# Kernel tuning notes

Hardware: AMD Instinct MI355X
Metric: run time of the kernel (lower is better)

## Reference

```python
import jax, jax.numpy as jnp
import numpy as np

D_MODEL = 1024
D_STATE = 16
D_CONV = 4
EXPAND = 2
D_INNER = EXPAND * D_MODEL
BATCH = 2
SEQ = 4096


def setup_inputs() -> dict:
    key = jax.random.key(0)
    ks = jax.random.split(key, 8)
    def w(k, shape, fan_in):
        return jax.random.normal(k, shape, jnp.float32) * (fan_in ** -0.5)
    x = jax.random.normal(ks[0], (BATCH, SEQ, D_MODEL), jnp.float32)
    in_proj_w = w(ks[1], (2 * D_INNER, D_MODEL), D_MODEL)
    conv_w = w(ks[2], (D_INNER, 1, D_CONV), D_CONV)          # depthwise conv kernel (OIH, groups=D_INNER)
    conv_b = jnp.zeros((D_INNER,), jnp.float32)
    x_proj_w = w(ks[3], (1 + 2 * D_STATE, D_INNER), D_INNER)
    dt_proj_w = w(ks[4], (D_INNER, 1), D_STATE)               # Linear(1 -> d_inner), see notes
    dt_proj_b = jnp.zeros((D_INNER,), jnp.float32)
    A_log = jnp.log(jnp.tile(jnp.arange(1, D_STATE + 1, dtype=jnp.float32)[None, :], (D_INNER, 1)))
    D = jnp.ones((D_INNER,), jnp.float32)
    out_proj_w = w(ks[5], (D_MODEL, D_INNER), D_INNER)
    return dict(x=x, in_proj_w=in_proj_w, conv_w=conv_w, conv_b=conv_b,
                x_proj_w=x_proj_w, dt_proj_w=dt_proj_w, dt_proj_b=dt_proj_b,
                A_log=A_log, D=D, out_proj_w=out_proj_w)


def _selective_scan(xs, delta, Bm, Cm, A, D):
    # xs, delta: [B, L, d_inner]; Bm, Cm: [B, L, d_state]; A: [d_inner, d_state]
    def step(h, inp):
        x_t, d_t, b_t, c_t = inp                      # [B,di],[B,di],[B,n],[B,n]
        dA = jnp.exp(d_t[..., None] * A)              # [B, di, n]
        h = dA * h + (d_t * x_t)[..., None] * b_t[:, None, :]
        y = jnp.einsum('bdn,bn->bd', h, c_t) + D * x_t
        return h, y
    h0 = jnp.zeros((xs.shape[0], xs.shape[2], A.shape[1]), xs.dtype)
    seq = (jnp.swapaxes(xs, 0, 1), jnp.swapaxes(delta, 0, 1),
           jnp.swapaxes(Bm, 0, 1), jnp.swapaxes(Cm, 0, 1))
    _, ys = jax.lax.scan(step, h0, seq)               # ys: [L, B, di]
    return jnp.swapaxes(ys, 0, 1)


def _mamba(x, in_proj_w, conv_w, conv_b, x_proj_w, dt_proj_w, dt_proj_b, A_log, D, out_proj_w):
    xz = x @ in_proj_w.T                               # [B, L, 2*di]
    xc, z = jnp.split(xz, 2, axis=-1)
    # causal depthwise conv (pad left d_conv-1, truncate to seq_len)
    u = jnp.swapaxes(xc, 1, 2)                         # [B, di, L]
    u = jax.lax.conv_general_dilated(
        u, conv_w, window_strides=(1,), padding=[(D_CONV - 1, 0)],
        feature_group_count=D_INNER, dimension_numbers=('NCH', 'OIH', 'NCH'))
    u = u + conv_b[None, :, None]
    xs = jax.nn.silu(jnp.swapaxes(u, 1, 2))            # [B, L, di]
    dbc = xs @ x_proj_w.T                              # [B, L, 1+2n]
    delta_raw = dbc[..., :1]
    Bm = dbc[..., 1:1 + D_STATE]
    Cm = dbc[..., 1 + D_STATE:]
    delta = jax.nn.softplus(delta_raw @ dt_proj_w.T + dt_proj_b)   # [B, L, di]
    A = -jnp.exp(A_log)
    y = _selective_scan(xs, delta, Bm, Cm, A, D)
    return (y * jax.nn.silu(z)) @ out_proj_w.T


def reference(x, in_proj_w, conv_w, conv_b, x_proj_w, dt_proj_w, dt_proj_b, A_log, D, out_proj_w):
    return _mamba(x, in_proj_w, conv_w, conv_b, x_proj_w, dt_proj_w, dt_proj_b, A_log, D, out_proj_w)
```

## Files before the change

kernel.cpp:

```cpp
#include <hip/hip_runtime.h>
#include <hip/hip_bf16.h>
#include <stdint.h>

typedef __bf16 bf16x8 __attribute__((ext_vector_type(8)));
typedef float  f32x4  __attribute__((ext_vector_type(4)));
typedef float  f32x2  __attribute__((ext_vector_type(2)));
typedef unsigned short u16x8 __attribute__((ext_vector_type(8)));

#define TC 32
#define NC 128
#define TH 16

__device__ __forceinline__ unsigned short f2bf(float f) {
  unsigned u = __builtin_bit_cast(unsigned, f);
  unsigned r = (u + 0x7fffu + ((u >> 16) & 1u)) >> 16;
  return (unsigned short)r;
}
__device__ __forceinline__ float bf2f(unsigned short s) {
  unsigned u = ((unsigned)s) << 16;
  return __builtin_bit_cast(float, u);
}

__device__ __forceinline__ void gload_lds16(const void* g, void* l) {
  __builtin_amdgcn_global_load_lds(
      (const __attribute__((address_space(1))) unsigned int*)(g),
      (__attribute__((address_space(3))) unsigned int*)(l),
      16, 0, 0);
}

__global__ __launch_bounds__(256) void prep_k(
    const float4* __restrict__ x, const float4* __restrict__ ipw,
    const float4* __restrict__ opw, const float* __restrict__ xpw,
    ushort4* __restrict__ xb, ushort4* __restrict__ wb1,
    ushort4* __restrict__ wb2, unsigned short* __restrict__ xwp)
{
  const int r = blockIdx.y;
  int i = blockIdx.x * 256 + threadIdx.x;
  const int stride = gridDim.x * 256;
  if (r == 0) {
    for (; i < 2097152; i += stride) {
      float4 v = x[i]; ushort4 o;
      o.x = f2bf(v.x); o.y = f2bf(v.y); o.z = f2bf(v.z); o.w = f2bf(v.w);
      xb[i] = o;
    }
  } else if (r == 1) {
    for (; i < 1048576; i += stride) {
      float4 v = ipw[i]; ushort4 o;
      o.x = f2bf(v.x); o.y = f2bf(v.y); o.z = f2bf(v.z); o.w = f2bf(v.w);
      wb1[i] = o;
    }
  } else if (r == 2) {
    for (; i < 524288; i += stride) {
      float4 v = opw[i]; ushort4 o;
      o.x = f2bf(v.x); o.y = f2bf(v.y); o.z = f2bf(v.z); o.w = f2bf(v.w);
      wb2[i] = o;
    }
  } else {
    for (; i < 262144; i += stride) {
      int row = i >> 11, col = i & 2047;
      xwp[i] = (row < 33) ? f2bf(xpw[row * 2048 + col]) : (unsigned short)0;
    }
  }
}

template <bool BF16OUT, bool SWZ>
__global__ __launch_bounds__(512) void gemm8p(
    const unsigned short* __restrict__ A, const unsigned short* __restrict__ B,
    void* __restrict__ Cv, int M, int N, int K)
{
  __shared__ __align__(16) unsigned short As[2][2][8192];
  __shared__ __align__(16) unsigned short Bs[2][2][8192];
  const int tid = threadIdx.x;

  const int grid_m = M >> 8, grid_n = N >> 8;
  const int nwg = grid_m * grid_n;
  int wid = blockIdx.x;
  if (SWZ) { int q = nwg >> 3; wid = (wid & 7) * q + (wid >> 3); }
  const int GM = 8;
  const int nig = GM * grid_n;
  const int gidg = wid / nig;
  const int rem = wid - gidg * nig;
  const int fm = gidg * GM;
  const int gsz = (grid_m - fm < GM) ? (grid_m - fm) : GM;
  const int pm = fm + rem % gsz;
  const int pn = rem / gsz;
  const int m0 = pm << 8, n0 = pn << 8;

  const int NT = K >> 6;

  const int wq = tid >> 6, l = tid & 63;
  const int wr2 = wq >> 2, wc2 = wq & 3;
  const int lr = l & 15, q16 = l >> 4;
  const int sw = lr & 7;

  const unsigned short* aH0 = A + (size_t)m0 * K;
  const unsigned short* aH1 = A + (size_t)(m0 + 128) * K;
  const unsigned short* bH0 = B + (size_t)n0 * K;
  const unsigned short* bH1 = B + (size_t)(n0 + 128) * K;

#define STAGE8(srcbase, dstp, kt)                                              \
  { _Pragma("unroll") for (int i = 0; i < 2; ++i) {                            \
      int q = tid + 512 * i; int rw = q >> 3; int ssl = (q & 7) ^ (rw & 7);    \
      gload_lds16((srcbase) + (size_t)rw * K + (size_t)(kt) * 64 + ssl * 8,    \
                  (dstp) + q * 8); } }

#define LDA(dd, MH)                                                            \
  { _Pragma("unroll") for (int mi = 0; mi < 4; ++mi) {                         \
      int ar = (wr2 * 64 + mi * 16 + lr) * 64;                                 \
      _Pragma("unroll") for (int ks = 0; ks < 2; ++ks)                         \
        af[mi][ks] = *(const bf16x8*)&As[dd][MH][ar + (((ks * 4 + q16) ^ sw) << 3)]; } }

#define LDB(dd, NH)                                                            \
  { _Pragma("unroll") for (int ni = 0; ni < 2; ++ni) {                         \
      int br = (wc2 * 32 + ni * 16 + lr) * 64;                                 \
      _Pragma("unroll") for (int ks = 0; ks < 2; ++ks)                         \
        bf2[NH][ni][ks] = *(const bf16x8*)&Bs[dd][NH][br + (((ks * 4 + q16) ^ sw) << 3)]; } }

#define MMA(MH, NH)                                                            \
  { __builtin_amdgcn_s_setprio(1);                                             \
    _Pragma("unroll") for (int mi = 0; mi < 4; ++mi)                           \
    _Pragma("unroll") for (int ni = 0; ni < 2; ++ni)                           \
    _Pragma("unroll") for (int ks = 0; ks < 2; ++ks)                           \
      acc[MH][NH][mi][ni] = __builtin_amdgcn_mfma_f32_16x16x32_bf16(           \
          af[mi][ks], bf2[NH][ni][ks], acc[MH][NH][mi][ni], 0, 0, 0);          \
    __builtin_amdgcn_s_setprio(0); }

  f32x4 acc[2][2][4][2];
#pragma unroll
  for (int a = 0; a < 2; ++a)
#pragma unroll
    for (int b = 0; b < 2; ++b)
#pragma unroll
      for (int c = 0; c < 4; ++c)
#pragma unroll
        for (int d = 0; d < 2; ++d)
          acc[a][b][c][d] = (f32x4){0.f, 0.f, 0.f, 0.f};

  bf16x8 af[4][2];
  bf16x8 bf2[2][2][2];

  STAGE8(aH0, As[0][0], 0);
  STAGE8(aH1, As[0][1], 0);
  STAGE8(bH0, Bs[0][0], 0);
  STAGE8(bH1, Bs[0][1], 0);
  asm volatile("s_waitcnt vmcnt(0)" ::: "memory");
  __builtin_amdgcn_s_barrier();

  for (int t = 0; t < NT; ++t) {
    const int d = t & 1;
    LDA(d, 0);
    LDB(d, 0);
    if (t + 1 < NT) {
      STAGE8(aH0, As[d ^ 1][0], t + 1);
      STAGE8(aH1, As[d ^ 1][1], t + 1);
      STAGE8(bH0, Bs[d ^ 1][0], t + 1);
      STAGE8(bH1, Bs[d ^ 1][1], t + 1);
    }
    MMA(0, 0);
    LDB(d, 1);
    MMA(0, 1);
    LDA(d, 1);
    MMA(1, 1);
    MMA(1, 0);
    asm volatile("s_waitcnt vmcnt(0)" ::: "memory");
    __builtin_amdgcn_s_barrier();
  }

#pragma unroll
  for (int mh = 0; mh < 2; ++mh)
#pragma unroll
    for (int nh = 0; nh < 2; ++nh)
#pragma unroll
      for (int mi = 0; mi < 4; ++mi)
#pragma unroll
        for (int ni = 0; ni < 2; ++ni) {
          int gr = m0 + mh * 128 + wr2 * 64 + mi * 16 + q16 * 4;
          int gc = n0 + nh * 128 + wc2 * 32 + ni * 16 + lr;
#pragma unroll
          for (int j = 0; j < 4; ++j) {
            if (BF16OUT)
              ((unsigned short*)Cv)[(size_t)(gr + j) * N + gc] = f2bf(acc[mh][nh][mi][ni][j]);
            else
              ((float*)Cv)[(size_t)(gr + j) * N + gc] = acc[mh][nh][mi][ni][j];
          }
        }
#undef STAGE8
#undef LDA
#undef LDB
#undef MMA
}

template <bool BF16OUT, bool SWZ>
__global__ __launch_bounds__(256) void gemm2p(
    const unsigned short* __restrict__ A, const unsigned short* __restrict__ B,
    void* __restrict__ Cv, int M, int N, int K)
{
  __shared__ __align__(16) unsigned short AsB[3 * 128 * 32];
  __shared__ __align__(16) unsigned short BsB[3 * 128 * 32];
  const int tid = threadIdx.x;

  const int grid_m = M >> 7, grid_n = N >> 7;
  const int nwg = grid_m * grid_n;
  int wid = blockIdx.x;
  if (SWZ) { int q = nwg >> 3; wid = (wid & 7) * q + (wid >> 3); }
  const int GM = 16;
  const int nig = GM * grid_n;
  const int gidg = wid / nig;
  const int rem = wid - gidg * nig;
  const int fm = gidg * GM;
  const int gsz = (grid_m - fm < GM) ? (grid_m - fm) : GM;
  const int pm = fm + rem % gsz;
  const int pn = rem / gsz;
  const int m0 = pm << 7, n0 = pn << 7;

  const int kseg = K / gridDim.z;
  const int kbeg = blockIdx.z * kseg;
  const int NT = kseg >> 5;

  const int w = tid >> 6, l = tid & 63;
  const int wr = w >> 1, wc = w & 1;
  const int lr = l & 15, kk = (l >> 4) * 8;

  f32x4 acc[4][4];
#pragma unroll
  for (int mi = 0; mi < 4; ++mi)
#pragma unroll
    for (int ni = 0; ni < 4; ++ni)
      acc[mi][ni] = (f32x4){0.f, 0.f, 0.f, 0.f};

#pragma unroll
  for (int tt = 0; tt < 2; ++tt) {
    unsigned short* as = AsB + tt * 4096;
    unsigned short* bs = BsB + tt * 4096;
    int k0 = kbeg + tt * 32;
#pragma unroll
    for (int i = 0; i < 2; ++i) {
      int q = tid + 256 * i;
      int row = q >> 2, sub = (q & 3) ^ ((q >> 3) & 3);
      gload_lds16(A + (size_t)(m0 + row) * K + k0 + sub * 8, as + q * 8);
      gload_lds16(B + (size_t)(n0 + row) * K + k0 + sub * 8, bs + q * 8);
    }
  }
  asm volatile("s_waitcnt vmcnt(4)\n\ts_barrier" ::: "memory");

  for (int t = 0; t < NT; ++t) {
    if (t + 2 < NT) {
      unsigned short* as = AsB + ((t + 2) % 3) * 4096;
      unsigned short* bs = BsB + ((t + 2) % 3) * 4096;
      int k0 = kbeg + (t + 2) * 32;
#pragma unroll
      for (int i = 0; i < 2; ++i) {
        int q = tid + 256 * i;
        int row = q >> 2, sub = (q & 3) ^ ((q >> 3) & 3);
        gload_lds16(A + (size_t)(m0 + row) * K + k0 + sub * 8, as + q * 8);
        gload_lds16(B + (size_t)(n0 + row) * K + k0 + sub * 8, bs + q * 8);
      }
    }
    const unsigned short* as = AsB + (t % 3) * 4096;
    const unsigned short* bs = BsB + (t % 3) * 4096;
    bf16x8 af[4], bfr[4];
#pragma unroll
    for (int mi = 0; mi < 4; ++mi) {
      int row = wr * 64 + mi * 16 + lr;
      int col = kk ^ (((row >> 1) & 3) << 3);
      af[mi] = *(const bf16x8*)&as[row * 32 + col];
    }
#pragma unroll
    for (int ni = 0; ni < 4; ++ni) {
      int row = wc * 64 + ni * 16 + lr;
      int col = kk ^ (((row >> 1) & 3) << 3);
      bfr[ni] = *(const bf16x8*)&bs[row * 32 + col];
    }
    __builtin_amdgcn_s_setprio(1);
#pragma unroll
    for (int mi = 0; mi < 4; ++mi)
#pragma unroll
      for (int ni = 0; ni < 4; ++ni)
        acc[mi][ni] = __builtin_amdgcn_mfma_f32_16x16x32_bf16(af[mi], bfr[ni], acc[mi][ni], 0, 0, 0);
    __builtin_amdgcn_s_setprio(0);
    if (t + 1 < NT) {
      if (t + 2 < NT) asm volatile("s_waitcnt vmcnt(4)\n\ts_barrier" ::: "memory");
      else            asm volatile("s_waitcnt vmcnt(0)\n\ts_barrier" ::: "memory");
    }
  }

#pragma unroll
  for (int mi = 0; mi < 4; ++mi)
#pragma unroll
    for (int ni = 0; ni < 4; ++ni) {
      int gr = m0 + wr * 64 + mi * 16 + (l >> 4) * 4;
      int gc = n0 + wc * 64 + ni * 16 + (l & 15);
#pragma unroll
      for (int j = 0; j < 4; ++j) {
        if (BF16OUT)
          ((unsigned short*)Cv)[(size_t)(gr + j) * N + gc] = f2bf(acc[mi][ni][j]);
        else
          ((float*)Cv + (size_t)blockIdx.z * M * N)[(size_t)(gr + j) * N + gc] = acc[mi][ni][j];
      }
    }
}

__global__ __launch_bounds__(256) void redux4_k(const float4* __restrict__ part,
                                                float4* __restrict__ out) {
  int i = blockIdx.x * 256 + threadIdx.x;
  const int STR = 262144;
  float4 a = part[i], b = part[i + STR], c = part[i + 2 * STR], d = part[i + 3 * STR];
  out[i] = make_float4(a.x + b.x + c.x + d.x, a.y + b.y + c.y + d.y,
                       a.z + b.z + c.z + d.z, a.w + b.w + c.w + d.w);
}

#define CONV_L 16
__global__ __launch_bounds__(256) void conv_silu_k(
    const unsigned short* __restrict__ xzb, const float* __restrict__ cw,
    const float* __restrict__ cb, unsigned short* __restrict__ xsb)
{
  const int b = blockIdx.y;
  const int l0 = blockIdx.x * CONV_L;
  const int d = threadIdx.x * 8;
  float w[4][8], bias[8];
#pragma unroll
  for (int i = 0; i < 8; ++i) {
    bias[i] = cb[d + i];
#pragma unroll
    for (int j = 0; j < 4; ++j) w[j][i] = cw[(d + i) * 4 + j];
  }
  const size_t rb = (size_t)b * 4096;
  float win[3][8];
#pragma unroll
  for (int j = 0; j < 3; ++j) {
    int l = l0 - 3 + j;
    if (l >= 0) {
      u16x8 v = *(const u16x8*)(xzb + (rb + l) * 4096 + d);
#pragma unroll
      for (int i = 0; i < 8; ++i) win[j][i] = bf2f(v[i]);
    } else {
#pragma unroll
      for (int i = 0; i < 8; ++i) win[j][i] = 0.f;
    }
  }
  for (int l = l0; l < l0 + CONV_L; ++l) {
    u16x8 v = *(const u16x8*)(xzb + (rb + l) * 4096 + d);
    float cur[8]; u16x8 ob;
#pragma unroll
    for (int i = 0; i < 8; ++i) {
      cur[i] = bf2f(v[i]);
      float u = bias[i] + w[0][i] * win[0][i] + w[1][i] * win[1][i]
                        + w[2][i] * win[2][i] + w[3][i] * cur[i];
      float s = u / (1.f + __expf(-u));
      ob[i] = f2bf(s);
    }
    *(u16x8*)(xsb + (rb + l) * 2048 + d) = ob;
#pragma unroll
    for (int i = 0; i < 8; ++i) { win[0][i] = win[1][i]; win[1][i] = win[2][i]; win[2][i] = cur[i]; }
  }
}

__global__ __launch_bounds__(256) void scan_p1(
    const unsigned short* __restrict__ xsb16, const float* __restrict__ dbc,
    const float* __restrict__ dtw, const float* __restrict__ dtb,
    const float* __restrict__ alog,
    float* __restrict__ Sg, float* __restrict__ cdg)
{
  const int chunk = blockIdx.x;
  const int d0 = blockIdx.y * 256;
  const int b = blockIdx.z;
  const int tid = threadIdx.x;
  const size_t rowbase = (size_t)b * 4096 + chunk * TC;

  __shared__ __align__(16) unsigned short xsS[TH][256];
  __shared__ __align__(16) float bS[TC][16];
  __shared__ float drS[TC];

  if (tid < TC) drS[tid] = dbc[(rowbase + tid) * 128];
  for (int i = tid; i < TC * 16; i += 256) {
    int t = i >> 4, q = i & 15;
    bS[t][q] = dbc[(rowbase + t) * 128 + 1 + q];
  }

  const int d = d0 + tid;
  const float wdt = dtw[d], bdt = dtb[d];
  float adn[16];
  bool ok = true;
#pragma unroll
  for (int k = 0; k < 4; ++k) {
    float4 a4 = *(const float4*)(alog + (size_t)d * 16 + k * 4);
    adn[4 * k + 0] = -__expf(a4.x); adn[4 * k + 1] = -__expf(a4.y);
    adn[4 * k + 2] = -__expf(a4.z); adn[4 * k + 3] = -__expf(a4.w);
  }
#pragma unroll
  for (int n = 0; n < 16; ++n)
    ok = ok && (fabsf(adn[n] + (float)(n + 1)) <= 1e-3f * (float)(n + 1));

  f32x2 h2[8];
#pragma unroll
  for (int k = 0; k < 8; ++k) h2[k] = (f32x2){0.f, 0.f};
  float cd = 0.f;

  for (int half = 0; half < 2; ++half) {
    if (half) __syncthreads();
    for (int i = tid; i < TH * 32; i += 256) {
      int tt = i >> 5, q = i & 31;
      *(u16x8*)&xsS[tt][q * 8] =
          *(const u16x8*)(xsb16 + (rowbase + half * TH + tt) * 2048 + d0 + q * 8);
    }
    __syncthreads();

    if (ok) {
      for (int tt = 0; tt < TH; ++tt) {
        int t = half * TH + tt;
        float pre = fmaf(drS[t], wdt, bdt);
        float e = __expf(pre);
        float dlt = (pre > 20.f) ? pre : __logf(1.f + e);
        float xv = bf2f(xsS[tt][tid]);
        float dx = dlt * xv;
        cd += dlt;
        float r = __expf(-dlt);
        float r2 = r * r;
        f32x2 s2 = (f32x2){r2, r2};
        f32x2 rp2[8];
        rp2[0] = (f32x2){r, r2};
#pragma unroll
        for (int k = 1; k < 8; ++k) rp2[k] = rp2[k - 1] * s2;
        f32x4 Bv[4];
#pragma unroll
        for (int k = 0; k < 4; ++k) Bv[k] = ((const f32x4*)&bS[t][0])[k];
        f32x2 dx2 = (f32x2){dx, dx};
#pragma unroll
        for (int k = 0; k < 4; ++k) {
          f32x2 blo = __builtin_shufflevector(Bv[k], Bv[k], 0, 1);
          f32x2 bhi = __builtin_shufflevector(Bv[k], Bv[k], 2, 3);
          h2[2 * k]     = rp2[2 * k]     * h2[2 * k]     + dx2 * blo;
          h2[2 * k + 1] = rp2[2 * k + 1] * h2[2 * k + 1] + dx2 * bhi;
        }
      }
    } else {
      for (int tt = 0; tt < TH; ++tt) {
        int t = half * TH + tt;
        float pre = fmaf(drS[t], wdt, bdt);
        float e = __expf(pre);
        float dlt = (pre > 20.f) ? pre : __logf(1.f + e);
        float xv = bf2f(xsS[tt][tid]);
        float dx = dlt * xv;
        cd += dlt;
        f32x4 Bv[4];
#pragma unroll
        for (int k = 0; k < 4; ++k) Bv[k] = ((const f32x4*)&bS[t][0])[k];
#pragma unroll
        for (int n = 0; n < 16; ++n) {
          float dA = __expf(adn[n] * dlt);
          h2[n >> 1][n & 1] = fmaf(dA, h2[n >> 1][n & 1], dx * Bv[n >> 2][n & 3]);
        }
      }
    }
  }
  cdg[(size_t)(b * NC + chunk) * 2048 + d] = cd;
  float* Sp = Sg + ((size_t)(b * NC + chunk) * 32768 + (size_t)d * 16);
#pragma unroll
  for (int k = 0; k < 4; ++k)
    ((float4*)Sp)[k] = make_float4(h2[2 * k][0], h2[2 * k][1], h2[2 * k + 1][0], h2[2 * k + 1][1]);
}

__global__ __launch_bounds__(256) void scan_p2(
    float* __restrict__ Sg, const float* __restrict__ cdg,
    const float* __restrict__ alog)
{
  int g = blockIdx.x * 256 + threadIdx.x;
  int b = g >> 15, dn = g & 32767;
  int d = dn >> 4;
  float adn = -__expf(alog[dn]);
  float h = 0.f;
  size_t o = (size_t)(b * NC) * 32768 + dn;
  size_t oc = (size_t)(b * NC) * 2048 + d;
  float S = Sg[o];
  float cdv = cdg[oc];
  for (int c = 0; c < NC; ++c) {
    float Sn = 0.f, cdn = 0.f;
    if (c + 1 < NC) {
      Sn = Sg[o + 32768];
      cdn = cdg[oc + 2048];
    }
    float P = __expf(adn * cdv);
    Sg[o] = h;
    h = fmaf(P, h, S);
    S = Sn; cdv = cdn;
    o += 32768; oc += 2048;
  }
}

__global__ __launch_bounds__(256) void scan_p3(
    const unsigned short* __restrict__ xsb16, const float* __restrict__ dbc,
    const float* __restrict__ dtw, const float* __restrict__ dtb,
    const float* __restrict__ alog, const float* __restrict__ Dp,
    const unsigned short* __restrict__ xzb, const float* __restrict__ Hg,
    unsigned short* __restrict__ gb)
{
  const int chunk = blockIdx.x;
  const int d0 = blockIdx.y * 256;
  const int b = blockIdx.z;
  const int tid = threadIdx.x;
  const size_t rowbase = (size_t)b * 4096 + chunk * TC;

  __shared__ __align__(16) unsigned short xsS[TH][256];
  __shared__ __align__(16) float bcS[TC][32];

  for (int i = tid; i < TC * 32; i += 256) {
    int t = i >> 5, q = i & 31;
    bcS[t][q] = dbc[(rowbase + t) * 128 + 1 + q];
  }

  const int d = d0 + tid;
  const float wdt = dtw[d], bdt = dtb[d], Dd = Dp[d];
  const float* __restrict__ drp = dbc + rowbase * 128;
  float adn[16];
  bool ok = true;
#pragma unroll
  for (int k = 0; k < 4; ++k) {
    float4 a4 = *(const float4*)(alog + (size_t)d * 16 + k * 4);
    adn[4 * k + 0] = -__expf(a4.x); adn[4 * k + 1] = -__expf(a4.y);
    adn[4 * k + 2] = -__expf(a4.z); adn[4 * k + 3] = -__expf(a4.w);
  }
#pragma unroll
  for (int n = 0; n < 16; ++n)
    ok = ok && (fabsf(adn[n] + (float)(n + 1)) <= 1e-3f * (float)(n + 1));

  f32x2 h2[8];
  {
    const float* Hp = Hg + ((size_t)(b * NC + chunk) * 32768 + (size_t)d * 16);
#pragma unroll
    for (int k = 0; k < 4; ++k) {
      float4 h4 = ((const float4*)Hp)[k];
      h2[2 * k]     = (f32x2){h4.x, h4.y};
      h2[2 * k + 1] = (f32x2){h4.z, h4.w};
    }
  }

  for (int half = 0; half < 2; ++half) {
    if (half) __syncthreads();
    for (int i = tid; i < TH * 32; i += 256) {
      int tt = i >> 5, q = i & 31;
      *(u16x8*)&xsS[tt][q * 8] =
          *(const u16x8*)(xsb16 + (rowbase + half * TH + tt) * 2048 + d0 + q * 8);
    }
    __syncthreads();

    if (ok) {
      for (int tt = 0; tt < TH; ++tt) {
        int t = half * TH + tt;
        float pre = fmaf(drp[(size_t)t * 128], wdt, bdt);
        float e = __expf(pre);
        float dlt = (pre > 20.f) ? pre : __logf(1.f + e);
        float xv = bf2f(xsS[tt][tid]);
        float dx = dlt * xv;
        float r = __expf(-dlt);
        float r2 = r * r;
        f32x2 s2 = (f32x2){r2, r2};
        f32x2 rp2[8];
        rp2[0] = (f32x2){r, r2};
#pragma unroll
        for (int k = 1; k < 8; ++k) rp2[k] = rp2[k - 1] * s2;
        f32x4 Bv[4], Cv[4];
#pragma unroll
        for (int k = 0; k < 4; ++k) {
          Bv[k] = ((const f32x4*)&bcS[t][0])[k];
          Cv[k] = ((const f32x4*)&bcS[t][16])[k];
        }
        f32x2 dx2 = (f32x2){dx, dx};
        f32x2 yp2[4];
#pragma unroll
        for (int k = 0; k < 4; ++k) yp2[k] = (f32x2){0.f, 0.f};
#pragma unroll
        for (int k = 0; k < 4; ++k) {
          f32x2 blo = __builtin_shufflevector(Bv[k], Bv[k], 0, 1);
          f32x2 bhi = __builtin_shufflevector(Bv[k], Bv[k], 2, 3);
          f32x2 clo = __builtin_shufflevector(Cv[k], Cv[k], 0, 1);
          f32x2 chi = __builtin_shufflevector(Cv[k], Cv[k], 2, 3);
          h2[2 * k]     = rp2[2 * k]     * h2[2 * k]     + dx2 * blo;
          h2[2 * k + 1] = rp2[2 * k + 1] * h2[2 * k + 1] + dx2 * bhi;
          yp2[k] = h2[2 * k] * clo + yp2[k];
          yp2[k] = h2[2 * k + 1] * chi + yp2[k];
        }
        f32x2 ys = (yp2[0] + yp2[1]) + (yp2[2] + yp2[3]);
        float y = ys[0] + ys[1] + Dd * xv;
        xsS[tt][tid] = f2bf(y);
      }
    } else {
      for (int tt = 0; tt < TH; ++tt) {
        int t = half * TH + tt;
        float pre = fmaf(drp[(size_t)t * 128], wdt, bdt);
        float e = __expf(pre);
        float dlt = (pre > 20.f) ? pre : __logf(1.f + e);
        float xv = bf2f(xsS[tt][tid]);
        float dx = dlt * xv;
        f32x4 Bv[4], Cv[4];
#pragma unroll
        for (int k = 0; k < 4; ++k) {
          Bv[k] = ((const f32x4*)&bcS[t][0])[k];
          Cv[k] = ((const f32x4*)&bcS[t][16])[k];
        }
        float yp[4];
        yp[0] = Dd * xv; yp[1] = 0.f; yp[2] = 0.f; yp[3] = 0.f;
#pragma unroll
        for (int n = 0; n < 16; ++n) {
          float dA = __expf(adn[n] * dlt);
          h2[n >> 1][n & 1] = fmaf(dA, h2[n >> 1][n & 1], dx * Bv[n >> 2][n & 3]);
          yp[n & 3] = fmaf(h2[n >> 1][n & 1], Cv[n >> 2][n & 3], yp[n & 3]);
        }
        float y = (yp[0] + yp[1]) + (yp[2] + yp[3]);
        xsS[tt][tid] = f2bf(y);
      }
    }
    __syncthreads();

    for (int i = tid; i < TH * 32; i += 256) {
      int tt = i >> 5, q = i & 31;
      size_t row = rowbase + half * TH + tt;
      u16x8 yv = *(const u16x8*)&xsS[tt][q * 8];
      u16x8 zv = *(const u16x8*)(xzb + row * 4096 + 2048 + d0 + q * 8);
      u16x8 ov;
#pragma unroll
      for (int j = 0; j < 8; ++j) {
        float z = bf2f(zv[j]);
        float s = z / (1.f + __expf(-z));
        ov[j] = f2bf(bf2f(yv[j]) * s);
      }
      *(u16x8*)(gb + row * 2048 + d0 + q * 8) = ov;
    }
  }
}

extern "C" void kernel_launch(void* const* d_in, const int* in_sizes, int n_in,
                              void* d_out, int out_size, void* d_ws, size_t ws_size,
                              hipStream_t stream) {
  const float* x    = (const float*)d_in[0];
  const float* ipw  = (const float*)d_in[1];
  const float* cw   = (const float*)d_in[2];
  const float* cb   = (const float*)d_in[3];
  const float* xpw  = (const float*)d_in[4];
  const float* dtw  = (const float*)d_in[5];
  const float* dtb  = (const float*)d_in[6];
  const float* alog = (const float*)d_in[7];
  const float* Dp   = (const float*)d_in[8];
  const float* opw  = (const float*)d_in[9];
  float* out = (float*)d_out;

  char* p = (char*)d_ws;
  unsigned short* xb   = (unsigned short*)p; p += (size_t)8388608 * 2;
  unsigned short* wb1  = (unsigned short*)p; p += (size_t)4194304 * 2;
  unsigned short* wb2  = (unsigned short*)p; p += (size_t)2097152 * 2;
  unsigned short* xwp  = (unsigned short*)p; p += (size_t)262144 * 2;
  unsigned short* xzb  = (unsigned short*)p; p += (size_t)33554432 * 2;
  unsigned short* xsb16= (unsigned short*)p; p += (size_t)16777216 * 2;
  float*          dbc  = (float*)p;          p += (size_t)1048576 * 4;
  unsigned short* gb   = (unsigned short*)p; p += (size_t)16777216 * 2;
  float*          Sg   = (float*)p;          p += (size_t)8388608 * 4;
  float*          cdg  = (float*)p;          p += (size_t)524288 * 4;
  float*          dbcp = Sg;

  prep_k<<<dim3(512, 4), 256, 0, stream>>>(
      (const float4*)x, (const float4*)ipw, (const float4*)opw, xpw,
      (ushort4*)xb, (ushort4*)wb1, (ushort4*)wb2, xwp);

  gemm8p<true, true><<<512, 512, 0, stream>>>(xb, wb1, xzb, 8192, 4096, 1024);
  conv_silu_k<<<dim3(4096 / CONV_L, 2), 256, 0, stream>>>(xzb, cw, cb, xsb16);

  gemm2p<false, false><<<dim3(64, 1, 4), 256, 0, stream>>>(xsb16, xwp, dbcp, 8192, 128, 2048);
  redux4_k<<<1024, 256, 0, stream>>>((const float4*)dbcp, (float4*)dbc);

  scan_p1<<<dim3(NC, 8, 2), 256, 0, stream>>>(xsb16, dbc, dtw, dtb, alog, Sg, cdg);
  scan_p2<<<256, 256, 0, stream>>>(Sg, cdg, alog);
  scan_p3<<<dim3(NC, 8, 2), 256, 0, stream>>>(xsb16, dbc, dtw, dtb, alog, Dp, xzb, Sg, gb);

  gemm2p<false, true><<<dim3(512, 1, 1), 256, 0, stream>>>(gb, wb2, out, 8192, 1024, 2048);
}
```

Baseline: 290.3 us.

## Rewrite in_proj GEMM with 16 waves per block and K=32 double buffering

Replaces the 8-wave 256x256 in_proj GEMM, which used a K=64 step and split half-tile loads into four MMA phases, with a 16-wave version. Each wave now owns a 64x64 output tile and the block steps through K in 32-wide slices with a new LDS swizzle. Per-wave register use and LDS footprint both drop, which should allow more waves in flight to hide latency. The cost is twice as many barriers per K and less register-level reuse of fragments per wave.

Result: slower. 299.1 us (+3.0%).

```diff
diff --git a/kernel.cpp b/kernel.cpp
--- a/kernel.cpp
+++ b/kernel.cpp
@@ -64,12 +64,12 @@
 }
 
 template <bool BF16OUT, bool SWZ>
-__global__ __launch_bounds__(512) void gemm8p(
+__global__ __launch_bounds__(1024, 4) void gemm16w(
     const unsigned short* __restrict__ A, const unsigned short* __restrict__ B,
     void* __restrict__ Cv, int M, int N, int K)
 {
-  __shared__ __align__(16) unsigned short As[2][2][8192];
-  __shared__ __align__(16) unsigned short Bs[2][2][8192];
+  __shared__ __align__(16) unsigned short As[2][8192];
+  __shared__ __align__(16) unsigned short Bs[2][8192];
   const int tid = threadIdx.x;
 
   const int grid_m = M >> 8, grid_n = N >> 8;
@@ -86,108 +86,79 @@
   const int pn = rem / gsz;
   const int m0 = pm << 8, n0 = pn << 8;
 
-  const int NT = K >> 6;
+  const int NT = K >> 5;
 
   const int wq = tid >> 6, l = tid & 63;
-  const int wr2 = wq >> 2, wc2 = wq & 3;
+  const int wrow = wq >> 2, wcol = wq & 3;
   const int lr = l & 15, q16 = l >> 4;
-  const int sw = lr & 7;
-
-  const unsigned short* aH0 = A + (size_t)m0 * K;
-  const unsigned short* aH1 = A + (size_t)(m0 + 128) * K;
-  const unsigned short* bH0 = B + (size_t)n0 * K;
-  const unsigned short* bH1 = B + (size_t)(n0 + 128) * K;
-
-#define STAGE8(srcbase, dstp, kt)                                              \
-  { _Pragma("unroll") for (int i = 0; i < 2; ++i) {                            \
-      int q = tid + 512 * i; int rw = q >> 3; int ssl = (q & 7) ^ (rw & 7);    \
-      gload_lds16((srcbase) + (size_t)rw * K + (size_t)(kt) * 64 + ssl * 8,    \
-                  (dstp) + q * 8); } }
-
-#define LDA(dd, MH)                                                            \
+
+#define STAGE16(srcbase, dstp, kt)                                             \
+  { int q = tid; int rw = q >> 2; int ssl = (q & 3) ^ ((q >> 3) & 3);          \
+    gload_lds16((srcbase) + (size_t)rw * K + (size_t)(kt) * 32 + ssl * 8,      \
+                (dstp) + q * 8); }
+
+#define LDA16(dd)                                                              \
   { _Pragma("unroll") for (int mi = 0; mi < 4; ++mi) {                         \
-      int ar = (wr2 * 64 + mi * 16 + lr) * 64;                                 \
-      _Pragma("unroll") for (int ks = 0; ks < 2; ++ks)                         \
-        af[mi][ks] = *(const bf16x8*)&As[dd][MH][ar + (((ks * 4 + q16) ^ sw) << 3)]; } }
-
-#define LDB(dd, NH)                                                            \
-  { _Pragma("unroll") for (int ni = 0; ni < 2; ++ni) {                         \
-      int br = (wc2 * 32 + ni * 16 + lr) * 64;                                 \
-      _Pragma("unroll") for (int ks = 0; ks < 2; ++ks)                         \
-        bf2[NH][ni][ks] = *(const bf16x8*)&Bs[dd][NH][br + (((ks * 4 + q16) ^ sw) << 3)]; } }
-
-#define MMA(MH, NH)                                                            \
-  { __builtin_amdgcn_s_setprio(1);                                             \
-    _Pragma("unroll") for (int mi = 0; mi < 4; ++mi)                           \
-    _Pragma("unroll") for (int ni = 0; ni < 2; ++ni)                           \
-    _Pragma("unroll") for (int ks = 0; ks < 2; ++ks)                           \
-      acc[MH][NH][mi][ni] = __builtin_amdgcn_mfma_f32_16x16x32_bf16(           \
-          af[mi][ks], bf2[NH][ni][ks], acc[MH][NH][mi][ni], 0, 0, 0);          \
-    __builtin_amdgcn_s_setprio(0); }
-
-  f32x4 acc[2][2][4][2];
-#pragma unroll
-  for (int a = 0; a < 2; ++a)
-#pragma unroll
-    for (int b = 0; b < 2; ++b)
-#pragma unroll
-      for (int c = 0; c < 4; ++c)
-#pragma unroll
-        for (int d = 0; d < 2; ++d)
-          acc[a][b][c][d] = (f32x4){0.f, 0.f, 0.f, 0.f};
-
-  bf16x8 af[4][2];
-  bf16x8 bf2[2][2][2];
-
-  STAGE8(aH0, As[0][0], 0);
-  STAGE8(aH1, As[0][1], 0);
-  STAGE8(bH0, Bs[0][0], 0);
-  STAGE8(bH1, Bs[0][1], 0);
+      int row = wrow * 64 + mi * 16 + lr;                                      \
+      int col = (q16 ^ ((row >> 1) & 3)) << 3;                                 \
+      af[mi] = *(const bf16x8*)&As[dd][row * 32 + col]; } }
+
+#define LDB16(dd)                                                              \
+  { _Pragma("unroll") for (int ni = 0; ni < 4; ++ni) {                         \
+      int row = wcol * 64 + ni * 16 + lr;                                      \
+      int col = (q16 ^ ((row >> 1) & 3)) << 3;                                 \
+      bfr[ni] = *(const bf16x8*)&Bs[dd][row * 32 + col]; } }
+
+  f32x4 acc[4][4];
+#pragma unroll
+  for (int mi = 0; mi < 4; ++mi)
+#pragma unroll
+    for (int ni = 0; ni < 4; ++ni)
+      acc[mi][ni] = (f32x4){0.f, 0.f, 0.f, 0.f};
+
+  bf16x8 af[4], bfr[4];
+
+  STAGE16(A + (size_t)m0 * K, As[0], 0);
+  STAGE16(B + (size_t)n0 * K, Bs[0], 0);
   asm volatile("s_waitcnt vmcnt(0)" ::: "memory");
   __builtin_amdgcn_s_barrier();
 
   for (int t = 0; t < NT; ++t) {
     const int d = t & 1;
-    LDA(d, 0);
-    LDB(d, 0);
+    LDA16(d);
+    LDB16(d);
     if (t + 1 < NT) {
-      STAGE8(aH0, As[d ^ 1][0], t + 1);
-      STAGE8(aH1, As[d ^ 1][1], t + 1);
-      STAGE8(bH0, Bs[d ^ 1][0], t + 1);
-      STAGE8(bH1, Bs[d ^ 1][1], t + 1);
-    }
-    MMA(0, 0);
-    LDB(d, 1);
-    MMA(0, 1);
-    LDA(d, 1);
-    MMA(1, 1);
-    MMA(1, 0);
+      STAGE16(A + (size_t)m0 * K, As[d ^ 1], t + 1);
+      STAGE16(B + (size_t)n0 * K, Bs[d ^ 1], t + 1);
+    }
+    __builtin_amdgcn_s_setprio(1);
+#pragma unroll
+    for (int mi = 0; mi < 4; ++mi)
+#pragma unroll
+      for (int ni = 0; ni < 4; ++ni)
+        acc[mi][ni] = __builtin_amdgcn_mfma_f32_16x16x32_bf16(af[mi], bfr[ni], acc[mi][ni], 0, 0, 0);
+    __builtin_amdgcn_s_setprio(0);
     asm volatile("s_waitcnt vmcnt(0)" ::: "memory");
     __builtin_amdgcn_s_barrier();
   }
 
 #pragma unroll
-  for (int mh = 0; mh < 2; ++mh)
-#pragma unroll
-    for (int nh = 0; nh < 2; ++nh)
-#pragma unroll
-      for (int mi = 0; mi < 4; ++mi)
-#pragma unroll
-        for (int ni = 0; ni < 2; ++ni) {
-          int gr = m0 + mh * 128 + wr2 * 64 + mi * 16 + q16 * 4;
-          int gc = n0 + nh * 128 + wc2 * 32 + ni * 16 + lr;
-#pragma unroll
-          for (int j = 0; j < 4; ++j) {
-            if (BF16OUT)
-              ((unsigned short*)Cv)[(size_t)(gr + j) * N + gc] = f2bf(acc[mh][nh][mi][ni][j]);
-            else
-              ((float*)Cv)[(size_t)(gr + j) * N + gc] = acc[mh][nh][mi][ni][j];
-          }
-        }
-#undef STAGE8
-#undef LDA
-#undef LDB
-#undef MMA
+  for (int mi = 0; mi < 4; ++mi)
+#pragma unroll
+    for (int ni = 0; ni < 4; ++ni) {
+      int gr = m0 + wrow * 64 + mi * 16 + q16 * 4;
+      int gc = n0 + wcol * 64 + ni * 16 + lr;
+#pragma unroll
+      for (int j = 0; j < 4; ++j) {
+        if (BF16OUT)
+          ((unsigned short*)Cv)[(size_t)(gr + j) * N + gc] = f2bf(acc[mi][ni][j]);
+        else
+          ((float*)Cv)[(size_t)(gr + j) * N + gc] = acc[mi][ni][j];
+      }
+    }
+#undef STAGE16
+#undef LDA16
+#undef LDB16
 }
 
 template <bool BF16OUT, bool SWZ>
@@ -660,7 +631,7 @@
       (const float4*)x, (const float4*)ipw, (const float4*)opw, xpw,
       (ushort4*)xb, (ushort4*)wb1, (ushort4*)wb2, xwp);
 
-  gemm8p<true, true><<<512, 512, 0, stream>>>(xb, wb1, xzb, 8192, 4096, 1024);
+  gemm16w<true, true><<<512, 1024, 0, stream>>>(xb, wb1, xzb, 8192, 4096, 1024);
   conv_silu_k<<<dim3(4096 / CONV_L, 2), 256, 0, stream>>>(xzb, cw, cb, xsb16);
 
   gemm2p<false, false><<<dim3(64, 1, 4), 256, 0, stream>>>(xsb16, xwp, dbcp, 8192, 128, 2048);
```
